# Kernel tuning notes

Hardware: AMD Instinct MI355X
Metric: run time of the kernel (lower is better)

## Reference

```python
import jax, jax.numpy as jnp
import numpy as np

N_NODES = 20000
N_EDGES = 160000
N_GRAPHS = 64
EMB_DIM = 16
N_BASIS = 16
MAX_RADIUS = 5.0
MUL_IN = 8   # output_size: multiplicity of scalar atom features
MUL_OUT = 4  # multiplicity per output irrep (4x0e + 4x1o + 4x2e -> dim 36)
W_NUMEL = 3 * MUL_IN * MUL_IN * MUL_OUT  # 768 per-edge tensor-product weights


def setup_inputs() -> dict:
    key = jax.random.key(0)
    ks = jax.random.split(key, 16)
    pos = jax.random.normal(ks[0], (N_NODES, 3), jnp.float32) * 3.0
    A = jax.random.randint(ks[1], (N_NODES,), 0, 10)
    batch = jnp.sort(jax.random.randint(ks[2], (N_NODES,), 0, N_GRAPHS))
    edge_src = jax.random.randint(ks[3], (N_EDGES,), 0, N_NODES)
    edge_dst = jax.random.randint(ks[4], (N_EDGES,), 0, N_NODES)
    edge_shifts = jnp.zeros((N_EDGES, 3), jnp.float32)
    cell = jnp.broadcast_to(jnp.eye(3, dtype=jnp.float32) * 10.0, (N_GRAPHS, 3, 3))
    emb_table = jax.random.normal(ks[5], (10, EMB_DIM), jnp.float32)
    fit_w1 = jax.random.normal(ks[6], (EMB_DIM, 64), jnp.float32) * (2.0 / EMB_DIM) ** 0.5
    fit_b1 = jnp.zeros((64,), jnp.float32)
    fit_w2 = jax.random.normal(ks[7], (64, 32), jnp.float32) * (2.0 / 64.0) ** 0.5
    fit_b2 = jnp.zeros((32,), jnp.float32)
    fit_w3 = jax.random.normal(ks[8], (32, MUL_IN), jnp.float32) * (2.0 / 32.0) ** 0.5
    fit_b3 = jnp.zeros((MUL_IN,), jnp.float32)
    fc_w1 = jax.random.normal(ks[9], (N_BASIS, 64), jnp.float32)
    fc_w2 = jax.random.normal(ks[10], (64, 64), jnp.float32)
    fc_w3 = jax.random.normal(ks[11], (64, 64), jnp.float32)
    fc_w4 = jax.random.normal(ks[12], (64, W_NUMEL), jnp.float32)
    return dict(pos=pos, A=A, batch=batch, edge_src=edge_src, edge_dst=edge_dst,
                edge_shifts=edge_shifts, cell=cell, emb_table=emb_table,
                fit_w1=fit_w1, fit_b1=fit_b1, fit_w2=fit_w2, fit_b2=fit_b2,
                fit_w3=fit_w3, fit_b3=fit_b3,
                fc_w1=fc_w1, fc_w2=fc_w2, fc_w3=fc_w3, fc_w4=fc_w4)


def _forward(pos, edge_shifts, cell, emb_table, fit_w1, fit_b1, fit_w2, fit_b2,
             fit_w3, fit_b3, fc_w1, fc_w2, fc_w3, fc_w4, A, batch, edge_src, edge_dst):
    E = edge_src.shape[0]
    # edge vectors with periodic shifts
    shift = jnp.einsum('ni,nij->nj', edge_shifts, cell[batch[edge_src]])
    ev = pos[edge_dst] - pos[edge_src] + shift                     # [E,3]
    r = jnp.sqrt(jnp.sum(ev * ev, axis=1))                         # [E]
    v = ev / jnp.maximum(r, 1e-9)[:, None]
    x, y, z = v[:, 0], v[:, 1], v[:, 2]
    # spherical harmonics lmax=2, normalize=True, 'component' normalization (e3nn order)
    sh0 = jnp.ones_like(x)                                         # [E]
    sh1 = jnp.sqrt(3.0) * jnp.stack([y, z, x], axis=-1)            # [E,3]
    s15 = jnp.sqrt(15.0); s5 = jnp.sqrt(5.0)
    sh2 = jnp.stack([s15 * x * y, s15 * y * z, (s5 / 2.0) * (3.0 * z * z - 1.0),
                     s15 * x * z, (s15 / 2.0) * (x * x - y * y)], axis=-1)  # [E,5]
    # node scalar features: embedding + fitnet MLP (SiLU)
    h = jax.nn.silu(emb_table[A] @ fit_w1 + fit_b1)
    h = jax.nn.silu(h @ fit_w2 + fit_b2)
    Ai = h @ fit_w3 + fit_b3                                       # [N, MUL_IN]
    # soft_one_hot_linspace(gaussian, cutoff=True) * sqrt(n_basis)
    centers = jnp.linspace(0.0, MAX_RADIUS, N_BASIS + 2)[1:-1]
    step = centers[1] - centers[0]
    rb = jnp.exp(-(((r[:, None] - centers) / step) ** 2)) / 1.12 * jnp.sqrt(jnp.float32(N_BASIS))
    # radial net -> per-edge tensor-product weights (e3nn FullyConnectedNet style, no bias)
    g = jax.nn.silu(rb @ fc_w1 / jnp.sqrt(jnp.float32(N_BASIS)))
    g = jax.nn.silu(g @ fc_w2 / 8.0)
    g = jax.nn.silu(g @ fc_w3 / 8.0)
    w = (g @ fc_w4 / 8.0).reshape(E, 3, MUL_IN, MUL_IN, MUL_OUT)   # [E,3 paths,u,v,w]
    # FullTensorProduct(Ai_src, sh) then FullyConnectedTensorProduct(., Ai_dst) with
    # per-edge weights; scalar x irrep paths factorize: out_l[e,w,m] = S_l[e,w]*sh_l[e,m]
    P = Ai[edge_src][:, :, None] * Ai[edge_dst][:, None, :]        # [E,u,v]
    S = jnp.einsum('euv,eluvw->elw', P, w) / jnp.float32(MUL_IN)   # path norm 1/sqrt(u*v)
    out0 = S[:, 0, :] * sh0[:, None]                               # [E,4]
    out1 = (S[:, 1, :, None] * sh1[:, None, :]).reshape(E, MUL_OUT * 3)
    out2 = (S[:, 2, :, None] * sh2[:, None, :]).reshape(E, MUL_OUT * 5)
    ef = jnp.concatenate([out0, out1, out2], axis=-1)              # [E,36]
    # scatter-mean to destination nodes
    cnt = jnp.clip(jax.ops.segment_sum(jnp.ones((E,), ef.dtype), edge_dst,
                                       num_segments=N_NODES), 1.0)
    return jax.ops.segment_sum(ef, edge_dst, num_segments=N_NODES) / cnt[:, None]


def reference(pos, A, batch, edge_src, edge_dst, edge_shifts, cell, emb_table,
              fit_w1, fit_b1, fit_w2, fit_b2, fit_w3, fit_b3,
              fc_w1, fc_w2, fc_w3, fc_w4):
    return _forward(pos, edge_shifts, cell, emb_table, fit_w1, fit_b1, fit_w2,
                    fit_b2, fit_w3, fit_b3, fc_w1, fc_w2, fc_w3, fc_w4,
                    A, batch, edge_src, edge_dst)
```

## Files before the change

kernel.cpp:

```cpp
#include <hip/hip_runtime.h>
#include <math.h>

#define N_NODES 20000
#define N_EDGES 160000

#define NBINS   512
#define BINS1   513
#define RMAX    7.5f

static const size_t OFF_EF  = 0;
static const size_t OFF_T   = OFF_EF  + (size_t)N_EDGES * 16 * 4;
static const size_t OFF_G   = OFF_T   + (size_t)100 * 64 * 12 * 4;
static const size_t OFF_SV  = OFF_G   + (size_t)64 * BINS1 * 4;
static const size_t OFF_NOFF= OFF_SV  + (size_t)100 * BINS1 * 12 * 4;
static const size_t OFF_NCNT= OFF_NOFF+ (size_t)(N_NODES + 1) * 4;
static const size_t OFF_RANK= OFF_NCNT+ (size_t)N_NODES * 4;

#define P1_T_BLOCKS  25
#define P1_G_BLOCKS  9
#define P1_H_BLOCKS  625
#define P1_GRID (P1_T_BLOCKS + P1_G_BLOCKS + P1_H_BLOCKS)
#define P2_SCAN_BLOCKS 79
#define P2_CHUNKS 9
#define P2_GRID (P2_SCAN_BLOCKS + 100 * P2_CHUNKS)

__device__ __forceinline__ float silu_f(float x) {
    return x / (1.0f + __expf(-x));
}

__global__ __launch_bounds__(256) void prep1_kernel(
        const float* __restrict__ emb,
        const float* __restrict__ fw1, const float* __restrict__ fb1,
        const float* __restrict__ fw2, const float* __restrict__ fb2,
        const float* __restrict__ fw3, const float* __restrict__ fb3,
        const float* __restrict__ fc_w1, const float* __restrict__ fc_w2,
        const float* __restrict__ fc_w3, const float* __restrict__ fc_w4,
        const int* __restrict__ edst,
        float* __restrict__ T, float* __restrict__ g_tT,
        int* __restrict__ cnt_i, int* __restrict__ rank_e) {
    __shared__ float smem[4096];
    int b = blockIdx.x;
    int tid = threadIdx.x;

    if (b < P1_T_BLOCKS) {
        float* h1s = smem;
        float* h2s = smem + 640;
        float* ai  = smem + 960;
        for (int idx = tid; idx < 640; idx += 256) {
            int t = idx >> 6, j = idx & 63;
            float acc = fb1[j];
            #pragma unroll
            for (int i = 0; i < 16; i++) acc += emb[t * 16 + i] * fw1[i * 64 + j];
            h1s[idx] = silu_f(acc);
        }
        __syncthreads();
        for (int idx = tid; idx < 320; idx += 256) {
            int t = idx >> 5, j = idx & 31;
            float acc = fb2[j];
            #pragma unroll
            for (int i = 0; i < 64; i++) acc += h1s[t * 64 + i] * fw2[i * 32 + j];
            h2s[idx] = silu_f(acc);
        }
        __syncthreads();
        if (tid < 80) {
            int t = tid >> 3, j = tid & 7;
            float acc = fb3[j];
            #pragma unroll
            for (int i = 0; i < 32; i++) acc += h2s[t * 32 + i] * fw3[i * 8 + j];
            ai[tid] = acc;
        }
        __syncthreads();

        int idx = b * 256 + tid;
        int pair = idx >> 6;
        int k = idx & 63;
        int ts = pair / 10, td = pair - ts * 10;
        float a[8], bb[8];
        #pragma unroll
        for (int i = 0; i < 8; i++) a[i] = ai[ts * 8 + i];
        #pragma unroll
        for (int i = 0; i < 8; i++) bb[i] = ai[td * 8 + i];
        float sv[12];
        #pragma unroll
        for (int i = 0; i < 12; i++) sv[i] = 0.0f;
        const float* wk = fc_w4 + k * 768;
        #pragma unroll 2
        for (int u = 0; u < 8; u++) {
            #pragma unroll
            for (int v = 0; v < 8; v++) {
                float ab = a[u] * bb[v];
                const float* wp = wk + u * 32 + v * 4;
                float4 w0 = *(const float4*)(wp);
                float4 w1 = *(const float4*)(wp + 256);
                float4 w2 = *(const float4*)(wp + 512);
                sv[0] += ab * w0.x; sv[1] += ab * w0.y; sv[2]  += ab * w0.z; sv[3]  += ab * w0.w;
                sv[4] += ab * w1.x; sv[5] += ab * w1.y; sv[6]  += ab * w1.z; sv[7]  += ab * w1.w;
                sv[8] += ab * w2.x; sv[9] += ab * w2.y; sv[10] += ab * w2.z; sv[11] += ab * w2.w;
            }
        }
        float* tp = T + pair * 768 + k * 12;
        #pragma unroll
        for (int j = 0; j < 12; j++) tp[j] = sv[j];
    } else if (b < P1_T_BLOCKS + P1_G_BLOCKS) {
        int lane = tid & 63;
        int wq = __builtin_amdgcn_readfirstlane(tid >> 6);
        int bin = (b - P1_T_BLOCKS) * 64 + lane;
        bool valid = (bin <= NBINS);
        float r = (float)bin * (RMAX / (float)NBINS);

        float rb[16];
        const float step = 5.0f / 17.0f;
        const float istep = 17.0f / 5.0f;
        const float rsc = 4.0f / 1.12f;
        #pragma unroll
        for (int i = 0; i < 16; i++) {
            float dd = (r - (float)(i + 1) * step) * istep;
            rb[i] = __expf(-dd * dd) * rsc;
        }

        #pragma unroll
        for (int jj = 0; jj < 16; jj++) {
            int j = wq * 16 + jj;
            float a0 = 0, a1 = 0, a2 = 0, a3 = 0;
            #pragma unroll
            for (int i = 0; i < 16; i += 4) {
                a0 += rb[i]     * fc_w1[(i)     * 64 + j];
                a1 += rb[i + 1] * fc_w1[(i + 1) * 64 + j];
                a2 += rb[i + 2] * fc_w1[(i + 2) * 64 + j];
                a3 += rb[i + 3] * fc_w1[(i + 3) * 64 + j];
            }
            smem[j * 64 + lane] = silu_f(((a0 + a1) + (a2 + a3)) * 0.25f);
        }
        __syncthreads();

        float acc[16];
        #pragma unroll
        for (int jj = 0; jj < 16; jj++) acc[jj] = 0.0f;
        #pragma unroll
        for (int c = 0; c < 4; c++) {
            float hc[16];
            #pragma unroll
            for (int i = 0; i < 16; i++) hc[i] = smem[(c * 16 + i) * 64 + lane];
            #pragma unroll
            for (int jj = 0; jj < 16; jj++) {
                int j = wq * 16 + jj;
                #pragma unroll
                for (int i = 0; i < 16; i++) acc[jj] += hc[i] * fc_w2[(c * 16 + i) * 64 + j];
            }
        }
        __syncthreads();
        #pragma unroll
        for (int jj = 0; jj < 16; jj++) smem[(wq * 16 + jj) * 64 + lane] = silu_f(acc[jj] * 0.125f);
        __syncthreads();

        #pragma unroll
        for (int jj = 0; jj < 16; jj++) acc[jj] = 0.0f;
        #pragma unroll
        for (int c = 0; c < 4; c++) {
            float hc[16];
            #pragma unroll
            for (int i = 0; i < 16; i++) hc[i] = smem[(c * 16 + i) * 64 + lane];
            #pragma unroll
            for (int jj = 0; jj < 16; jj++) {
                int j = wq * 16 + jj;
                #pragma unroll
                for (int i = 0; i < 16; i++) acc[jj] += hc[i] * fc_w3[(c * 16 + i) * 64 + j];
            }
        }
        if (valid) {
            #pragma unroll
            for (int jj = 0; jj < 16; jj++)
                g_tT[(size_t)(wq * 16 + jj) * BINS1 + bin] = silu_f(acc[jj] * 0.125f);
        }
    } else {
        int e = (b - P1_T_BLOCKS - P1_G_BLOCKS) * 256 + tid;
        if (e < N_EDGES) rank_e[e] = atomicAdd(&cnt_i[edst[e]], 1);
    }
}

__global__ __launch_bounds__(256) void prep2_kernel(
        const int* __restrict__ cnt_i, int* __restrict__ node_off,
        const float* __restrict__ T, const float* __restrict__ g_tT,
        float* __restrict__ sv_table) {
    __shared__ float smem[4096];
    int b = blockIdx.x;
    int tid = threadIdx.x;

    if (b < P2_SCAN_BLOCKS) {
        int* wred = (int*)smem;
        int* wsum = (int*)smem + 4;
        int lane = tid & 63, w = tid >> 6;
        int nbase = b * 256;
        int n = nbase + tid;
        int c = (n < N_NODES) ? cnt_i[n] : 0;

        int part = 0;
        for (int i = tid; i < nbase; i += 256) part += cnt_i[i];
        #pragma unroll
        for (int off = 1; off < 64; off <<= 1) part += __shfl_xor(part, off);
        if (lane == 0) wred[w] = part;

        int sc = c;
        #pragma unroll
        for (int off = 1; off < 64; off <<= 1) {
            int v2 = __shfl_up(sc, off);
            if (lane >= off) sc += v2;
        }
        if (lane == 63) wsum[w] = sc;
        __syncthreads();

        int base = wred[0] + wred[1] + wred[2] + wred[3];
        int wb = 0;
        #pragma unroll
        for (int i = 0; i < 4; i++) wb += (i < w) ? wsum[i] : 0;
        if (n < N_NODES) node_off[n] = base + wb + (sc - c);
        if (b == 0 && tid == 0) node_off[N_NODES] = N_EDGES;
        return;
    }

    int idx = b - P2_SCAN_BLOCKS;
    int pair = idx / P2_CHUNKS;
    int chunk = idx - pair * P2_CHUNKS;

    float* part = smem;
    float* Tlds = smem + 3328;

    const float* Tp = T + pair * 768;
    #pragma unroll
    for (int i = tid; i < 768; i += 256) Tlds[i] = Tp[i];
    __syncthreads();

    int lane = tid & 63;
    int wq = tid >> 6;
    int bin = chunk * 64 + lane;
    bool valid = (bin <= NBINS);
    int rb = valid ? bin : NBINS;

    float acc[12];
    #pragma unroll
    for (int j = 0; j < 12; j++) acc[j] = 0.0f;
    #pragma unroll
    for (int kk = 0; kk < 16; kk++) {
        int k = wq * 16 + kk;
        float g = g_tT[(size_t)k * BINS1 + rb];
        const float* Tl = Tlds + k * 12;
        #pragma unroll
        for (int j = 0; j < 12; j++) acc[j] += g * Tl[j];
    }

    float* pp = part + (size_t)wq * 64 * 13 + (size_t)lane * 13;
    #pragma unroll
    for (int j = 0; j < 12; j++) pp[j] = acc[j];
    __syncthreads();

    const float isc = 1.0f / 64.0f;
    float* svp = sv_table + (size_t)pair * BINS1 * 12 + (size_t)chunk * 64 * 12;
    #pragma unroll
    for (int i = 0; i < 3; i++) {
        int o = tid + 256 * i;
        int bl = o / 12;
        int j = o - bl * 12;
        if (chunk * 64 + bl <= NBINS) {
            float s = part[(size_t)0 * 832 + bl * 13 + j]
                    + part[(size_t)1 * 832 + bl * 13 + j]
                    + part[(size_t)2 * 832 + bl * 13 + j]
                    + part[(size_t)3 * 832 + bl * 13 + j];
            svp[o] = s * isc;
        }
    }
}

__global__ __launch_bounds__(256) void edge_table_kernel(
        const float* __restrict__ pos, const int* __restrict__ batch,
        const int* __restrict__ esrc, const int* __restrict__ edst,
        const float* __restrict__ shifts, const float* __restrict__ cell,
        const int* __restrict__ A,
        const int* __restrict__ node_off, const int* __restrict__ rank_e,
        const float* __restrict__ sv_table, float* __restrict__ ef) {
    int e = blockIdx.x * 256 + threadIdx.x;
    if (e >= N_EDGES) return;

    int s = esrc[e], d = edst[e];
    int slot = rank_e[e];
    int base = node_off[d];

    int gb = batch[s];
    float t0 = shifts[e * 3 + 0], t1 = shifts[e * 3 + 1], t2 = shifts[e * 3 + 2];
    const float* C = cell + gb * 9;
    float shx = t0 * C[0] + t1 * C[3] + t2 * C[6];
    float shy = t0 * C[1] + t1 * C[4] + t2 * C[7];
    float shz = t0 * C[2] + t1 * C[5] + t2 * C[8];
    float ex = pos[d * 3 + 0] - pos[s * 3 + 0] + shx;
    float ey = pos[d * 3 + 1] - pos[s * 3 + 1] + shy;
    float ez = pos[d * 3 + 2] - pos[s * 3 + 2] + shz;
    float r = sqrtf(ex * ex + ey * ey + ez * ez);
    float inv = 1.0f / fmaxf(r, 1e-9f);
    float x = ex * inv, y = ey * inv, z = ez * inv;

    float sv[12];
    if (r >= RMAX) {
        #pragma unroll
        for (int j = 0; j < 12; j++) sv[j] = 0.0f;
    } else {
        int pair = A[s] * 10 + A[d];
        float t = r * ((float)NBINS / RMAX);
        int i = (int)t;
        i = (i > NBINS - 1) ? (NBINS - 1) : i;
        float f = t - (float)i;
        const float* r0 = sv_table + ((size_t)pair * BINS1 + i) * 12;
        #pragma unroll
        for (int j = 0; j < 12; j++) {
            float lo = r0[j], hi = r0[12 + j];
            sv[j] = lo + f * (hi - lo);
        }
    }

    float4* dst = (float4*)(ef + (size_t)(base + slot) * 16);
    dst[0] = make_float4(sv[0], sv[1], sv[2],  sv[3]);
    dst[1] = make_float4(sv[4], sv[5], sv[6],  sv[7]);
    dst[2] = make_float4(sv[8], sv[9], sv[10], sv[11]);
    dst[3] = make_float4(x, y, z, 0.0f);
}

__global__ __launch_bounds__(256) void gather_kernel(const float* __restrict__ ef,
                                                     const int* __restrict__ node_off,
                                                     float* __restrict__ out) {
    int t = blockIdx.x * 256 + threadIdx.x;
    if (t >= N_NODES * 8) return;
    int n = t >> 3;
    int q = t & 7;
    int beg = node_off[n], end = node_off[n + 1];
    const float4* ef4 = (const float4*)ef;

    const float S3  = 1.7320508075688772f;
    const float S15 = 3.8729833462074170f;
    const float S5  = 2.2360679774997896f;

    float acc[36];
    #pragma unroll
    for (int j = 0; j < 36; j++) acc[j] = 0.0f;

    for (int p = beg + q; p < end; p += 8) {
        const float4* rp = ef4 + (size_t)p * 4;
        float4 svA = rp[0];
        float4 svB = rp[1];
        float4 svC = rp[2];
        float4 dv  = rp[3];
        float x = dv.x, y = dv.y, z = dv.z;
        float sh1v[3] = { S3 * y, S3 * z, S3 * x };
        float sh2v[5] = { S15 * x * y, S15 * y * z, 0.5f * S5 * (3.0f * z * z - 1.0f),
                          S15 * x * z, 0.5f * S15 * (x * x - y * y) };
        acc[0] += svA.x; acc[1] += svA.y; acc[2] += svA.z; acc[3] += svA.w;
        float bw[4] = { svB.x, svB.y, svB.z, svB.w };
        #pragma unroll
        for (int w = 0; w < 4; w++) {
            #pragma unroll
            for (int j = 0; j < 3; j++) acc[4 + w * 3 + j] += bw[w] * sh1v[j];
        }
        float cw[4] = { svC.x, svC.y, svC.z, svC.w };
        #pragma unroll
        for (int w = 0; w < 4; w++) {
            #pragma unroll
            for (int j = 0; j < 5; j++) acc[16 + w * 5 + j] += cw[w] * sh2v[j];
        }
    }

    #pragma unroll
    for (int j = 0; j < 36; j++) {
        acc[j] += __shfl_xor(acc[j], 1);
        acc[j] += __shfl_xor(acc[j], 2);
        acc[j] += __shfl_xor(acc[j], 4);
    }

    if (q == 0) {
        float c = 1.0f / fmaxf((float)(end - beg), 1.0f);
        float4* o4 = (float4*)out + (size_t)n * 9;
        #pragma unroll
        for (int k = 0; k < 9; k++)
            o4[k] = make_float4(acc[k * 4 + 0] * c, acc[k * 4 + 1] * c,
                                acc[k * 4 + 2] * c, acc[k * 4 + 3] * c);
    }
}

extern "C" void kernel_launch(void* const* d_in, const int* in_sizes, int n_in,
                              void* d_out, int out_size, void* d_ws, size_t ws_size,
                              hipStream_t stream) {
    const float* pos    = (const float*)d_in[0];
    const int*   A      = (const int*)d_in[1];
    const int*   batch  = (const int*)d_in[2];
    const int*   esrc   = (const int*)d_in[3];
    const int*   edst   = (const int*)d_in[4];
    const float* shifts = (const float*)d_in[5];
    const float* cell   = (const float*)d_in[6];
    const float* emb    = (const float*)d_in[7];
    const float* fw1    = (const float*)d_in[8];
    const float* fb1    = (const float*)d_in[9];
    const float* fw2    = (const float*)d_in[10];
    const float* fb2    = (const float*)d_in[11];
    const float* fw3    = (const float*)d_in[12];
    const float* fb3    = (const float*)d_in[13];
    const float* fcw1   = (const float*)d_in[14];
    const float* fcw2   = (const float*)d_in[15];
    const float* fcw3   = (const float*)d_in[16];
    const float* fcw4   = (const float*)d_in[17];
    float* out = (float*)d_out;

    char* ws = (char*)d_ws;
    float* ef      = (float*)(ws + OFF_EF);
    float* T       = (float*)(ws + OFF_T);
    float* g_tT    = (float*)(ws + OFF_G);
    float* sv_table= (float*)(ws + OFF_SV);
    int*   node_off= (int*)(ws + OFF_NOFF);
    int*   cnt_i   = (int*)(ws + OFF_NCNT);
    int*   rank_e  = (int*)(ws + OFF_RANK);

    hipMemsetAsync(cnt_i, 0, (size_t)N_NODES * 4, stream);

    prep1_kernel<<<P1_GRID, 256, 0, stream>>>(emb, fw1, fb1, fw2, fb2, fw3, fb3,
                                              fcw1, fcw2, fcw3, fcw4, edst,
                                              T, g_tT, cnt_i, rank_e);
    prep2_kernel<<<P2_GRID, 256, 0, stream>>>(cnt_i, node_off, T, g_tT, sv_table);
    edge_table_kernel<<<(N_EDGES + 255) / 256, 256, 0, stream>>>(
        pos, batch, esrc, edst, shifts, cell, A, node_off, rank_e, sv_table, ef);
    gather_kernel<<<(N_NODES * 8 + 255) / 256, 256, 0, stream>>>(ef, node_off, out);
}
```

Baseline: 159.1 us.

## Fuse per-edge feature computation into gather via CSR edge-id list

Replaces the edge_table kernel, which wrote a 64-byte per-edge feature record into CSR order, with a small kernel that writes only the edge id into CSR order. The gather kernel now recomputes the edge vector, radius and table interpolation inline for each incoming edge. This removes the write and re-read of the per-edge feature buffer. In exchange it adds indirect gathers of esrc, shifts, pos, batch, A and sv_table inside the gather loop, where the accesses are less coalesced.

```diff
diff --git a/kernel.cpp b/kernel.cpp
--- a/kernel.cpp
+++ b/kernel.cpp
@@ -8,13 +8,13 @@
 #define BINS1   513
 #define RMAX    7.5f
 
-static const size_t OFF_EF  = 0;
-static const size_t OFF_T   = OFF_EF  + (size_t)N_EDGES * 16 * 4;
+static const size_t OFF_T   = 0;
 static const size_t OFF_G   = OFF_T   + (size_t)100 * 64 * 12 * 4;
 static const size_t OFF_SV  = OFF_G   + (size_t)64 * BINS1 * 4;
 static const size_t OFF_NOFF= OFF_SV  + (size_t)100 * BINS1 * 12 * 4;
 static const size_t OFF_NCNT= OFF_NOFF+ (size_t)(N_NODES + 1) * 4;
 static const size_t OFF_RANK= OFF_NCNT+ (size_t)N_NODES * 4;
+static const size_t OFF_CSR = OFF_RANK+ (size_t)N_EDGES * 4;
 
 #define P1_T_BLOCKS  25
 #define P1_G_BLOCKS  9
@@ -270,67 +270,28 @@
     }
 }
 
-__global__ __launch_bounds__(256) void edge_table_kernel(
-        const float* __restrict__ pos, const int* __restrict__ batch,
-        const int* __restrict__ esrc, const int* __restrict__ edst,
-        const float* __restrict__ shifts, const float* __restrict__ cell,
-        const int* __restrict__ A,
-        const int* __restrict__ node_off, const int* __restrict__ rank_e,
-        const float* __restrict__ sv_table, float* __restrict__ ef) {
+__global__ __launch_bounds__(256) void csr_kernel(
+        const int* __restrict__ edst, const int* __restrict__ rank_e,
+        const int* __restrict__ node_off, int* __restrict__ csr_eid) {
     int e = blockIdx.x * 256 + threadIdx.x;
     if (e >= N_EDGES) return;
-
-    int s = esrc[e], d = edst[e];
-    int slot = rank_e[e];
-    int base = node_off[d];
-
-    int gb = batch[s];
-    float t0 = shifts[e * 3 + 0], t1 = shifts[e * 3 + 1], t2 = shifts[e * 3 + 2];
-    const float* C = cell + gb * 9;
-    float shx = t0 * C[0] + t1 * C[3] + t2 * C[6];
-    float shy = t0 * C[1] + t1 * C[4] + t2 * C[7];
-    float shz = t0 * C[2] + t1 * C[5] + t2 * C[8];
-    float ex = pos[d * 3 + 0] - pos[s * 3 + 0] + shx;
-    float ey = pos[d * 3 + 1] - pos[s * 3 + 1] + shy;
-    float ez = pos[d * 3 + 2] - pos[s * 3 + 2] + shz;
-    float r = sqrtf(ex * ex + ey * ey + ez * ez);
-    float inv = 1.0f / fmaxf(r, 1e-9f);
-    float x = ex * inv, y = ey * inv, z = ez * inv;
-
-    float sv[12];
-    if (r >= RMAX) {
-        #pragma unroll
-        for (int j = 0; j < 12; j++) sv[j] = 0.0f;
-    } else {
-        int pair = A[s] * 10 + A[d];
-        float t = r * ((float)NBINS / RMAX);
-        int i = (int)t;
-        i = (i > NBINS - 1) ? (NBINS - 1) : i;
-        float f = t - (float)i;
-        const float* r0 = sv_table + ((size_t)pair * BINS1 + i) * 12;
-        #pragma unroll
-        for (int j = 0; j < 12; j++) {
-            float lo = r0[j], hi = r0[12 + j];
-            sv[j] = lo + f * (hi - lo);
-        }
-    }
-
-    float4* dst = (float4*)(ef + (size_t)(base + slot) * 16);
-    dst[0] = make_float4(sv[0], sv[1], sv[2],  sv[3]);
-    dst[1] = make_float4(sv[4], sv[5], sv[6],  sv[7]);
-    dst[2] = make_float4(sv[8], sv[9], sv[10], sv[11]);
-    dst[3] = make_float4(x, y, z, 0.0f);
-}
-
-__global__ __launch_bounds__(256) void gather_kernel(const float* __restrict__ ef,
-                                                     const int* __restrict__ node_off,
-                                                     float* __restrict__ out) {
+    csr_eid[node_off[edst[e]] + rank_e[e]] = e;
+}
+
+__global__ __launch_bounds__(256) void gather_kernel(
+        const float* __restrict__ pos, const int* __restrict__ batch,
+        const int* __restrict__ esrc, const float* __restrict__ shifts,
+        const float* __restrict__ cell, const int* __restrict__ A,
+        const int* __restrict__ node_off, const int* __restrict__ csr_eid,
+        const float* __restrict__ sv_table, float* __restrict__ out) {
     int t = blockIdx.x * 256 + threadIdx.x;
     if (t >= N_NODES * 8) return;
     int n = t >> 3;
     int q = t & 7;
     int beg = node_off[n], end = node_off[n + 1];
-    const float4* ef4 = (const float4*)ef;
+
+    float pdx = pos[n * 3 + 0], pdy = pos[n * 3 + 1], pdz = pos[n * 3 + 2];
+    int Ad = A[n];
 
     const float S3  = 1.7320508075688772f;
     const float S15 = 3.8729833462074170f;
@@ -341,27 +302,55 @@
     for (int j = 0; j < 36; j++) acc[j] = 0.0f;
 
     for (int p = beg + q; p < end; p += 8) {
-        const float4* rp = ef4 + (size_t)p * 4;
-        float4 svA = rp[0];
-        float4 svB = rp[1];
-        float4 svC = rp[2];
-        float4 dv  = rp[3];
-        float x = dv.x, y = dv.y, z = dv.z;
+        int e = csr_eid[p];
+        int s = esrc[e];
+        int gb = batch[s];
+        float t0 = shifts[e * 3 + 0], t1 = shifts[e * 3 + 1], t2 = shifts[e * 3 + 2];
+        const float* C = cell + gb * 9;
+        float shx = t0 * C[0] + t1 * C[3] + t2 * C[6];
+        float shy = t0 * C[1] + t1 * C[4] + t2 * C[7];
+        float shz = t0 * C[2] + t1 * C[5] + t2 * C[8];
+        float ex = pdx - pos[s * 3 + 0] + shx;
+        float ey = pdy - pos[s * 3 + 1] + shy;
+        float ez = pdz - pos[s * 3 + 2] + shz;
+        float r = sqrtf(ex * ex + ey * ey + ez * ez);
+        float inv = 1.0f / fmaxf(r, 1e-9f);
+        float x = ex * inv, y = ey * inv, z = ez * inv;
+
+        float sv[12];
+        if (r >= RMAX) {
+            #pragma unroll
+            for (int j = 0; j < 12; j++) sv[j] = 0.0f;
+        } else {
+            int pair = A[s] * 10 + Ad;
+            float tt = r * ((float)NBINS / RMAX);
+            int i = (int)tt;
+            i = (i > NBINS - 1) ? (NBINS - 1) : i;
+            float f = tt - (float)i;
+            const float* r0 = sv_table + ((size_t)pair * BINS1 + i) * 12;
+            #pragma unroll
+            for (int j = 0; j < 12; j++) {
+                float lo = r0[j], hi = r0[12 + j];
+                sv[j] = lo + f * (hi - lo);
+            }
+        }
+
         float sh1v[3] = { S3 * y, S3 * z, S3 * x };
         float sh2v[5] = { S15 * x * y, S15 * y * z, 0.5f * S5 * (3.0f * z * z - 1.0f),
                           S15 * x * z, 0.5f * S15 * (x * x - y * y) };
-        acc[0] += svA.x; acc[1] += svA.y; acc[2] += svA.z; acc[3] += svA.w;
-        float bw[4] = { svB.x, svB.y, svB.z, svB.w };
+
+        acc[0] += sv[0]; acc[1] += sv[1]; acc[2] += sv[2]; acc[3] += sv[3];
         #pragma unroll
         for (int w = 0; w < 4; w++) {
-            #pragma unroll
-            for (int j = 0; j < 3; j++) acc[4 + w * 3 + j] += bw[w] * sh1v[j];
-        }
-        float cw[4] = { svC.x, svC.y, svC.z, svC.w };
+            float sw = sv[4 + w];
+            #pragma unroll
+            for (int j = 0; j < 3; j++) acc[4 + w * 3 + j] += sw * sh1v[j];
+        }
         #pragma unroll
         for (int w = 0; w < 4; w++) {
-            #pragma unroll
-            for (int j = 0; j < 5; j++) acc[16 + w * 5 + j] += cw[w] * sh2v[j];
+            float sw = sv[8 + w];
+            #pragma unroll
+            for (int j = 0; j < 5; j++) acc[16 + w * 5 + j] += sw * sh2v[j];
         }
     }
 
@@ -406,13 +395,13 @@
     float* out = (float*)d_out;
 
     char* ws = (char*)d_ws;
-    float* ef      = (float*)(ws + OFF_EF);
     float* T       = (float*)(ws + OFF_T);
     float* g_tT    = (float*)(ws + OFF_G);
     float* sv_table= (float*)(ws + OFF_SV);
     int*   node_off= (int*)(ws + OFF_NOFF);
     int*   cnt_i   = (int*)(ws + OFF_NCNT);
     int*   rank_e  = (int*)(ws + OFF_RANK);
+    int*   csr_eid = (int*)(ws + OFF_CSR);
 
     hipMemsetAsync(cnt_i, 0, (size_t)N_NODES * 4, stream);
 
@@ -420,7 +409,7 @@
                                               fcw1, fcw2, fcw3, fcw4, edst,
                                               T, g_tT, cnt_i, rank_e);
     prep2_kernel<<<P2_GRID, 256, 0, stream>>>(cnt_i, node_off, T, g_tT, sv_table);
-    edge_table_kernel<<<(N_EDGES + 255) / 256, 256, 0, stream>>>(
-        pos, batch, esrc, edst, shifts, cell, A, node_off, rank_e, sv_table, ef);
-    gather_kernel<<<(N_NODES * 8 + 255) / 256, 256, 0, stream>>>(ef, node_off, out);
-}
+    csr_kernel<<<(N_EDGES + 255) / 256, 256, 0, stream>>>(edst, rank_e, node_off, csr_eid);
+    gather_kernel<<<(N_NODES * 8 + 255) / 256, 256, 0, stream>>>(
+        pos, batch, esrc, shifts, cell, A, node_off, csr_eid, sv_table, out);
+}
```

Measured after the change: 157.3 us. Within noise of the previous version (-1.1%).
